# Optimization experiments

Measured on AMD Instinct MI355X. Metric: run time of the kernel, lower is better.

Reference implementation:

```python
import jax, jax.numpy as jnp
import numpy as np

N_NODES = 20000
E_RAND = 300000
IN_F, OUT_F, HEADS = 1280, 128, 4
HID = OUT_F * HEADS  # 512


def gat_conv(x, src, dst, W, attn_l, attn_r, bias, n_nodes):
    """DGL GATConv: fc (no bias) -> per-edge LeakyReLU(el_src+er_dst) ->
    segment softmax over incoming edges -> weighted scatter-sum -> +bias.
    Returns (N, HEADS, OUT_F)."""
    h = (x @ W).reshape(n_nodes, HEADS, OUT_F)            # (N,H,F)
    el = jnp.einsum('nhf,hf->nh', h, attn_l)              # (N,H)
    er = jnp.einsum('nhf,hf->nh', h, attn_r)              # (N,H)
    e = jax.nn.leaky_relu(el[src] + er[dst], 0.2)         # (E,H)
    emax = jax.ops.segment_max(e, dst, num_segments=n_nodes)
    ee = jnp.exp(e - emax[dst])                           # (E,H)
    denom = jax.ops.segment_sum(ee, dst, num_segments=n_nodes)
    alpha = ee / denom[dst]                               # (E,H)
    msg = h[src] * alpha[:, :, None]                      # (E,H,F)
    out = jax.ops.segment_sum(msg, dst, num_segments=n_nodes)
    return out + bias.reshape(HEADS, OUT_F)


def setup_inputs() -> dict:
    key = jax.random.key(0)
    ks = jax.random.split(key, 12)
    src_r = jax.random.randint(ks[0], (E_RAND,), 0, N_NODES)
    dst_r = jax.random.randint(ks[1], (E_RAND,), 0, N_NODES)
    self_loop = jnp.arange(N_NODES)
    src = jnp.concatenate([src_r, self_loop])  # self loops: contact[i][i]=1
    dst = jnp.concatenate([dst_r, self_loop])
    feature = jax.random.normal(ks[2], (N_NODES, IN_F), dtype=jnp.float32)
    s1 = 1.0 / np.sqrt(IN_F)
    s2 = 1.0 / np.sqrt(HID)
    return {
        'feature': feature,
        'W1': jax.random.normal(ks[3], (IN_F, HID), dtype=jnp.float32) * s1,
        'al1': jax.random.normal(ks[4], (HEADS, OUT_F), dtype=jnp.float32) * s2,
        'ar1': jax.random.normal(ks[5], (HEADS, OUT_F), dtype=jnp.float32) * s2,
        'b1': jnp.zeros((HID,), dtype=jnp.float32),
        'W2': jax.random.normal(ks[6], (HID, HID), dtype=jnp.float32) * s2,
        'al2': jax.random.normal(ks[7], (HEADS, OUT_F), dtype=jnp.float32) * s2,
        'ar2': jax.random.normal(ks[8], (HEADS, OUT_F), dtype=jnp.float32) * s2,
        'b2': jnp.zeros((HID,), dtype=jnp.float32),
        'Wfc': jax.random.normal(ks[9], (HID, 64), dtype=jnp.float32) * s2,
        'bfc': jnp.zeros((64,), dtype=jnp.float32),
        'src': src,
        'dst': dst,
    }


def reference(feature, W1, al1, ar1, b1, W2, al2, ar2, b2, Wfc, bfc, src, dst):
    n = feature.shape[0]
    out = gat_conv(feature, src, dst, W1, al1, ar1, b1, n)   # (N,4,128)
    out = jax.nn.elu(out).reshape(n, HID)                    # (N,512)
    out = gat_conv(out, src, dst, W2, al2, ar2, b2, n)       # (N,4,128)
    out = jax.nn.elu(out).reshape(n, HID)                    # (N,512)
    out = out @ Wfc + bfc                                    # (N,64)
    out = jax.nn.elu(out[None, :, :])                        # (1,N,64)
    return out
```

## Files before the change

### kernel.cpp

```cpp
#include <hip/hip_runtime.h>
#include <hip/hip_bf16.h>
#include <math.h>

#define HID 512
#define HEADS 4
#define OUTF 128

typedef __attribute__((ext_vector_type(8))) _Float16 f16x8_t;
typedef __attribute__((ext_vector_type(4))) _Float16 f16x4_t;
typedef __attribute__((ext_vector_type(4))) float f32x4_t;

__device__ __forceinline__ void gl_lds16(const void* g, void* l) {
    __builtin_amdgcn_global_load_lds(
        (const __attribute__((address_space(1))) void*)g,
        (__attribute__((address_space(3))) void*)l, 16, 0, 0);
}

__device__ __forceinline__ void stage_plane32(const _Float16* g, int strideE,
    int rbase, int rmax, char* plane, int wave, int lane)
{
    int gci = wave * 64 + lane;
    int r = gci >> 2, c = gci & 3;
    int rg = rbase + r; if (rg > rmax) rg = rmax;
    const char* s = (const char*)(g + (size_t)rg * strideE) + ((c ^ ((r >> 1) & 3)) << 4);
    char* d = plane + wave * 1024;
    gl_lds16(s, d);
}

__global__ __launch_bounds__(256) void conv16_kernel(const float* __restrict__ in,
    _Float16* __restrict__ o, int nquad)
{
    int stride = gridDim.x * 256;
    for (int i = blockIdx.x * 256 + threadIdx.x; i < nquad; i += stride) {
        float4 v = *(const float4*)&in[(size_t)i * 4];
        f16x4_t ov;
        ov[0] = (_Float16)v.x; ov[1] = (_Float16)v.y;
        ov[2] = (_Float16)v.z; ov[3] = (_Float16)v.w;
        *(f16x4_t*)&o[(size_t)i * 4] = ov;
    }
}

__global__ __launch_bounds__(256) void prep_w(const float* __restrict__ W,
    _Float16* __restrict__ Wt, int K, int NC)
{
    __shared__ float tile[32][33];
    const int k0 = blockIdx.x * 32, n0 = blockIdx.y * 32;
    const int t = threadIdx.x;
    {
        int r = t >> 3, c4 = (t & 7) * 4;
        float4 v = *(const float4*)&W[(size_t)(k0 + r) * NC + n0 + c4];
        tile[r][c4] = v.x; tile[r][c4 + 1] = v.y;
        tile[r][c4 + 2] = v.z; tile[r][c4 + 3] = v.w;
    }
    __syncthreads();
    int n = t >> 3, kc = (t & 7) * 4;
#pragma unroll
    for (int i = 0; i < 4; ++i)
        Wt[(size_t)(n0 + n) * K + k0 + kc + i] = (_Float16)tile[kc + i][n];
}

template<int EPI, int OUT16, int ELER>
__global__ __launch_bounds__(512, 6) void gemm_f16(
    const _Float16* __restrict__ Af, const _Float16* __restrict__ Bt,
    const float* __restrict__ bias,
    const float* __restrict__ attl, const float* __restrict__ attr,
    float* __restrict__ elp, float* __restrict__ erp,
    void* __restrict__ Cout, int M, int K, int NCOL, int ldC)
{
    __shared__ char lds[32768];
    const int tid = threadIdx.x;
    const int wave = tid >> 6, lane = tid & 63;
    const int wm = wave >> 2, wn = wave & 3;
    const int bm = blockIdx.y * 128, bn = blockIdx.x * 128;
    const int l15 = lane & 15, l4 = lane >> 4;
    const int swz = (l15 >> 1) & 3;

    f32x4_t acc[4][2];
#pragma unroll
    for (int i = 0; i < 4; ++i)
#pragma unroll
        for (int j = 0; j < 2; ++j) acc[i][j] = (f32x4_t){0.f, 0.f, 0.f, 0.f};

    const int nt = K >> 5;
    stage_plane32(Af, K, bm, M - 1, lds, wave, lane);
    stage_plane32(Bt, K, bn, NCOL - 1, lds + 8192, wave, lane);
    __syncthreads();

    for (int t = 0; t < nt; ++t) {
        char* AH = lds + (t & 1) * 16384;
        char* BH = AH + 8192;
        if (t + 1 < nt) {
            char* AHn = lds + ((t + 1) & 1) * 16384;
            stage_plane32(Af + (t + 1) * 32, K, bm, M - 1, AHn, wave, lane);
            stage_plane32(Bt + (t + 1) * 32, K, bn, NCOL - 1, AHn + 8192, wave, lane);
        }
        f16x8_t fa[4], fb[2];
#pragma unroll
        for (int mf = 0; mf < 4; ++mf) {
            int row = wm * 64 + mf * 16 + l15;
            fa[mf] = *(const f16x8_t*)(AH + row * 64 + ((l4 ^ swz) << 4));
        }
#pragma unroll
        for (int nf = 0; nf < 2; ++nf) {
            int rn = wn * 32 + nf * 16 + l15;
            fb[nf] = *(const f16x8_t*)(BH + rn * 64 + ((l4 ^ swz) << 4));
        }
#pragma unroll
        for (int mf = 0; mf < 4; ++mf)
#pragma unroll
            for (int nf = 0; nf < 2; ++nf)
                acc[mf][nf] = __builtin_amdgcn_mfma_f32_16x16x32_f16(fa[mf], fb[nf], acc[mf][nf], 0, 0, 0);
        __syncthreads();
    }
#pragma unroll
    for (int mf = 0; mf < 4; ++mf) {
        int rbase = bm + wm * 64 + mf * 16 + l4 * 4;
#pragma unroll
        for (int nf = 0; nf < 2; ++nf) {
            int col = bn + wn * 32 + nf * 16 + l15;
            if (col >= NCOL) continue;
#pragma unroll
            for (int r = 0; r < 4; ++r) {
                int row = rbase + r;
                if (row < M) {
                    float v = acc[mf][nf][r];
                    if (EPI) {
                        v += bias[col];
                        v = v > 0.f ? v : (expf(v) - 1.f);
                    }
                    if (OUT16) ((_Float16*)Cout)[(size_t)row * ldC + col] = (_Float16)v;
                    else       ((float*)Cout)[(size_t)row * ldC + col] = v;
                }
            }
        }
    }
    if (ELER) {
        const int head = blockIdx.x;
        float alv[2], arv[2];
#pragma unroll
        for (int nf = 0; nf < 2; ++nf) {
            int cl = wn * 32 + nf * 16 + l15;
            alv[nf] = attl[head * OUTF + cl];
            arv[nf] = attr[head * OUTF + cl];
        }
        float pel[4][4], perr[4][4];
#pragma unroll
        for (int mf = 0; mf < 4; ++mf)
#pragma unroll
            for (int r = 0; r < 4; ++r) {
                float se = 0.f, sr = 0.f;
#pragma unroll
                for (int nf = 0; nf < 2; ++nf) {
                    se = fmaf(acc[mf][nf][r], alv[nf], se);
                    sr = fmaf(acc[mf][nf][r], arv[nf], sr);
                }
                pel[mf][r] = se; perr[mf][r] = sr;
            }
#pragma unroll
        for (int off = 1; off < 16; off <<= 1)
#pragma unroll
            for (int mf = 0; mf < 4; ++mf)
#pragma unroll
                for (int r = 0; r < 4; ++r) {
                    pel[mf][r]  += __shfl_xor(pel[mf][r],  off);
                    perr[mf][r] += __shfl_xor(perr[mf][r], off);
                }
        __syncthreads();
        float* red = (float*)lds;
        if (l15 == 0) {
#pragma unroll
            for (int mf = 0; mf < 4; ++mf)
#pragma unroll
                for (int r = 0; r < 4; ++r) {
                    int rl = wm * 64 + mf * 16 + l4 * 4 + r;
                    red[rl * 4 + wn]       = pel[mf][r];
                    red[512 + rl * 4 + wn] = perr[mf][r];
                }
        }
        __syncthreads();
        if (tid < 128) {
            int row = bm + tid;
            if (row < M) {
                float es = red[tid * 4] + red[tid * 4 + 1] + red[tid * 4 + 2] + red[tid * 4 + 3];
                float rs = red[512 + tid * 4] + red[512 + tid * 4 + 1]
                         + red[512 + tid * 4 + 2] + red[512 + tid * 4 + 3];
                elp[row * HEADS + head] = es;
                erp[row * HEADS + head] = rs;
            }
        }
    }
}

__global__ void hist_kernel(const int* __restrict__ dst, int* __restrict__ deg, int E)
{
    int e = blockIdx.x * 256 + threadIdx.x;
    if (e < E) atomicAdd(&deg[dst[e]], 1);
}

__global__ __launch_bounds__(256) void scan1_kernel(const int* __restrict__ deg,
    int* __restrict__ offs, int* __restrict__ bsum, int N)
{
    __shared__ int buf[256];
    int tid = threadIdx.x;
    int i = blockIdx.x * 256 + tid;
    int v = (i < N) ? deg[i] : 0;
    buf[tid] = v;
    __syncthreads();
#pragma unroll
    for (int off = 1; off < 256; off <<= 1) {
        int t = (tid >= off) ? buf[tid - off] : 0;
        __syncthreads();
        buf[tid] += t;
        __syncthreads();
    }
    if (i < N) offs[i] = buf[tid] - v;
    if (tid == 255) bsum[blockIdx.x] = buf[255];
}

__global__ void scan2_kernel(int* __restrict__ bsum, int nb)
{
    if (threadIdx.x == 0) {
        int acc = 0;
        for (int b = 0; b < nb; ++b) { int t = bsum[b]; bsum[b] = acc; acc += t; }
        bsum[nb] = acc;
    }
}

__global__ void scan3_kernel(int* __restrict__ offs, const int* __restrict__ bsum,
                             int N, int nb)
{
    int i = blockIdx.x * 256 + threadIdx.x;
    if (i < N) offs[i] += bsum[blockIdx.x];
    if (i == 0) offs[N] = bsum[nb];
}

__global__ void fill_kernel(const int* __restrict__ srcv, const int* __restrict__ dstv,
    const int* __restrict__ offs, int* __restrict__ cursor,
    int* __restrict__ psrc, int E)
{
    int e = blockIdx.x * 256 + threadIdx.x;
    if (e < E) {
        int d = dstv[e];
        int p = atomicAdd(&cursor[d], 1);
        psrc[offs[d] + p] = srcv[e];
    }
}

__global__ __launch_bounds__(64) void aggregate_kernel(const _Float16* __restrict__ h,
    const int* __restrict__ offs, const int* __restrict__ psrc,
    const float* __restrict__ el, const float* __restrict__ er,
    const float* __restrict__ bias, _Float16* __restrict__ xo, int N)
{
    __shared__ int ssm[64];
    __shared__ float wsm[4][64];
    int n = blockIdx.x;
    int lane = threadIdx.x;
    int c = lane * 8;
    int head = lane >> 4;
    float4 erv = *(const float4*)&er[n * HEADS];
    float acc[8];
#pragma unroll
    for (int k = 0; k < 8; ++k) acc[k] = 0.f;
    float ws = 0.f;
    int beg = offs[n], end = offs[n + 1];
    for (int base = beg; base < end; base += 64) {
        int cnt = min(64, end - base);
        if (lane < cnt) {
            int s = psrc[base + lane];
            float4 lv = *(const float4*)&el[s * HEADS];
            float x;
            x = lv.x + erv.x; x = x > 0.f ? x : 0.2f * x; wsm[0][lane] = expf(x);
            x = lv.y + erv.y; x = x > 0.f ? x : 0.2f * x; wsm[1][lane] = expf(x);
            x = lv.z + erv.z; x = x > 0.f ? x : 0.2f * x; wsm[2][lane] = expf(x);
            x = lv.w + erv.w; x = x > 0.f ? x : 0.2f * x; wsm[3][lane] = expf(x);
            ssm[lane] = s;
        }
        __syncthreads();
        int j = 0;
        for (; j + 4 <= cnt; j += 4) {
            int s0 = ssm[j], s1 = ssm[j + 1], s2 = ssm[j + 2], s3 = ssm[j + 3];
            float w0 = wsm[head][j],     w1 = wsm[head][j + 1];
            float w2 = wsm[head][j + 2], w3 = wsm[head][j + 3];
            f16x8_t v0 = *(const f16x8_t*)&h[(size_t)s0 * HID + c];
            f16x8_t v1 = *(const f16x8_t*)&h[(size_t)s1 * HID + c];
            f16x8_t v2 = *(const f16x8_t*)&h[(size_t)s2 * HID + c];
            f16x8_t v3 = *(const f16x8_t*)&h[(size_t)s3 * HID + c];
#pragma unroll
            for (int k = 0; k < 8; ++k) {
                acc[k] = fmaf(w0, (float)v0[k], acc[k]);
                acc[k] = fmaf(w1, (float)v1[k], acc[k]);
                acc[k] = fmaf(w2, (float)v2[k], acc[k]);
                acc[k] = fmaf(w3, (float)v3[k], acc[k]);
            }
            ws += w0 + w1 + w2 + w3;
        }
        for (; j < cnt; ++j) {
            int s0 = ssm[j];
            float w0 = wsm[head][j];
            f16x8_t v0 = *(const f16x8_t*)&h[(size_t)s0 * HID + c];
#pragma unroll
            for (int k = 0; k < 8; ++k) acc[k] = fmaf(w0, (float)v0[k], acc[k]);
            ws += w0;
        }
        __syncthreads();
    }
    float inv = 1.f / ws;
    float4 b0 = *(const float4*)&bias[c];
    float4 b1 = *(const float4*)&bias[c + 4];
    float bb[8] = {b0.x, b0.y, b0.z, b0.w, b1.x, b1.y, b1.z, b1.w};
    f16x8_t ov;
#pragma unroll
    for (int k = 0; k < 8; ++k) {
        float r = acc[k] * inv + bb[k];
        r = r > 0.f ? r : (expf(r) - 1.f);
        ov[k] = (_Float16)r;
    }
    *(f16x8_t*)&xo[(size_t)n * HID + c] = ov;
}

extern "C" void kernel_launch(void* const* d_in, const int* in_sizes, int n_in,
                              void* d_out, int out_size, void* d_ws, size_t ws_size,
                              hipStream_t stream)
{
    const float* feature = (const float*)d_in[0];
    const float* W1  = (const float*)d_in[1];
    const float* al1 = (const float*)d_in[2];
    const float* ar1 = (const float*)d_in[3];
    const float* b1  = (const float*)d_in[4];
    const float* W2  = (const float*)d_in[5];
    const float* al2 = (const float*)d_in[6];
    const float* ar2 = (const float*)d_in[7];
    const float* b2  = (const float*)d_in[8];
    const float* Wfc = (const float*)d_in[9];
    const float* bfc = (const float*)d_in[10];
    const int* src = (const int*)d_in[11];
    const int* dst = (const int*)d_in[12];
    const int N = in_sizes[0] / 1280;
    const int E = in_sizes[11];
    const int nb = (N + 255) / 256;
    float* out = (float*)d_out;

    char* ws = (char*)d_ws;
    size_t off = 0;
    auto alloc = [&](size_t bytes) {
        void* p = ws + off;
        off += (bytes + 255) & ~(size_t)255;
        return p;
    };
    int* deg    = (int*)alloc((size_t)N * 4);
    int* cursor = (int*)alloc((size_t)N * 4);
    int* offs   = (int*)alloc((size_t)(N + 1) * 4);
    int* bsum   = (int*)alloc((size_t)(nb + 1) * 4);
    float* el   = (float*)alloc((size_t)N * HEADS * 4);
    float* er   = (float*)alloc((size_t)N * HEADS * 4);
    int* psrc   = (int*)alloc((size_t)E * 4);
    _Float16* featf = (_Float16*)alloc((size_t)N * 1280 * 2);
    _Float16* hbuf  = (_Float16*)alloc((size_t)N * HID * 2);
    _Float16* xh    = (_Float16*)alloc((size_t)N * HID * 2);
    _Float16* W1t   = (_Float16*)alloc((size_t)HID * 1280 * 2);
    _Float16* W2t   = (_Float16*)alloc((size_t)HID * HID * 2);
    _Float16* Wft   = (_Float16*)alloc((size_t)64 * HID * 2);

    hipMemsetAsync(deg, 0, (size_t)N * 4, stream);
    hipMemsetAsync(cursor, 0, (size_t)N * 4, stream);
    hist_kernel<<<(E + 255) / 256, 256, 0, stream>>>(dst, deg, E);
    scan1_kernel<<<nb, 256, 0, stream>>>(deg, offs, bsum, N);
    scan2_kernel<<<1, 64, 0, stream>>>(bsum, nb);
    scan3_kernel<<<nb, 256, 0, stream>>>(offs, bsum, N, nb);
    fill_kernel<<<(E + 255) / 256, 256, 0, stream>>>(src, dst, offs, cursor, psrc, E);

    conv16_kernel<<<2048, 256, 0, stream>>>(feature, featf, N * 1280 / 4);
    prep_w<<<dim3(1280 / 32, HID / 32), 256, 0, stream>>>(W1, W1t, 1280, HID);
    prep_w<<<dim3(HID / 32, HID / 32), 256, 0, stream>>>(W2, W2t, HID, HID);
    prep_w<<<dim3(HID / 32, 64 / 32), 256, 0, stream>>>(Wfc, Wft, HID, 64);

    dim3 ggrid(HID / 128, (N + 127) / 128);
    dim3 fgrid(1, (N + 127) / 128);

    gemm_f16<0, 1, 1><<<ggrid, 512, 0, stream>>>(featf, W1t, nullptr,
                                                 al1, ar1, el, er,
                                                 hbuf, N, 1280, HID, HID);
    aggregate_kernel<<<N, 64, 0, stream>>>(hbuf, offs, psrc, el, er, b1, xh, N);

    gemm_f16<0, 1, 1><<<ggrid, 512, 0, stream>>>(xh, W2t, nullptr,
                                                 al2, ar2, el, er,
                                                 hbuf, N, HID, HID, HID);
    aggregate_kernel<<<N, 64, 0, stream>>>(hbuf, offs, psrc, el, er, b2, xh, N);

    gemm_f16<1, 0, 0><<<fgrid, 512, 0, stream>>>(xh, Wft, bfc,
                                                 nullptr, nullptr, nullptr, nullptr,
                                                 out, N, HID, 64, 64);
}
```

Baseline: 276.1 us.

## Use 4-wave GEMM blocks with 64x64 warp tiles and XCD-aware block remapping

Switches the f16 GEMM from 8 waves per 128x128 tile to 4 waves, each computing a 64x64 sub-tile (4x4 MFMA fragments). Each wave reuses its fragments across more MFMAs and the block issues fewer LDS reads. The grid is also flattened to 1D and block IDs are remapped so consecutive logical tiles land on the same XCD, which should improve L2 reuse of shared A rows across the column tiles. In exchange it uses more accumulator registers per thread and fewer waves per CU to hide latency.

```diff
diff --git a/kernel.cpp b/kernel.cpp
--- a/kernel.cpp
+++ b/kernel.cpp
@@ -17,14 +17,17 @@
 }
 
 __device__ __forceinline__ void stage_plane32(const _Float16* g, int strideE,
-    int rbase, int rmax, char* plane, int wave, int lane)
-{
-    int gci = wave * 64 + lane;
-    int r = gci >> 2, c = gci & 3;
-    int rg = rbase + r; if (rg > rmax) rg = rmax;
-    const char* s = (const char*)(g + (size_t)rg * strideE) + ((c ^ ((r >> 1) & 3)) << 4);
-    char* d = plane + wave * 1024;
-    gl_lds16(s, d);
+    int rbase, int rmax, char* plane, int tid)
+{
+#pragma unroll
+    for (int j = 0; j < 2; ++j) {
+        int gci = j * 256 + tid;
+        int r = gci >> 2, c = gci & 3;
+        int rg = rbase + r; if (rg > rmax) rg = rmax;
+        const char* s = (const char*)(g + (size_t)rg * strideE) + ((c ^ ((r >> 1) & 3)) << 4);
+        char* d = plane + (j * 256 + (tid & ~63)) * 16;
+        gl_lds16(s, d);
+    }
 }
 
 __global__ __launch_bounds__(256) void conv16_kernel(const float* __restrict__ in,
@@ -60,30 +63,36 @@
 }
 
 template<int EPI, int OUT16, int ELER>
-__global__ __launch_bounds__(512, 6) void gemm_f16(
+__global__ __launch_bounds__(256, 3) void gemm_f16(
     const _Float16* __restrict__ Af, const _Float16* __restrict__ Bt,
     const float* __restrict__ bias,
     const float* __restrict__ attl, const float* __restrict__ attr,
     float* __restrict__ elp, float* __restrict__ erp,
-    void* __restrict__ Cout, int M, int K, int NCOL, int ldC)
+    void* __restrict__ Cout, int M, int K, int NCOL, int ldC,
+    int ncolT, int nwg)
 {
     __shared__ char lds[32768];
     const int tid = threadIdx.x;
     const int wave = tid >> 6, lane = tid & 63;
-    const int wm = wave >> 2, wn = wave & 3;
-    const int bm = blockIdx.y * 128, bn = blockIdx.x * 128;
+    const int wm = wave >> 1, wn = wave & 1;
+    const int b = blockIdx.x;
+    const int q = nwg >> 3, rr = nwg & 7;
+    const int xcd = b & 7, ib = b >> 3;
+    const int logical = (xcd < rr ? xcd * (q + 1) : rr * (q + 1) + (xcd - rr) * q) + ib;
+    const int bm = (logical / ncolT) * 128, bcol = logical % ncolT;
+    const int bn = bcol * 128;
     const int l15 = lane & 15, l4 = lane >> 4;
     const int swz = (l15 >> 1) & 3;
 
-    f32x4_t acc[4][2];
+    f32x4_t acc[4][4];
 #pragma unroll
     for (int i = 0; i < 4; ++i)
 #pragma unroll
-        for (int j = 0; j < 2; ++j) acc[i][j] = (f32x4_t){0.f, 0.f, 0.f, 0.f};
+        for (int j = 0; j < 4; ++j) acc[i][j] = (f32x4_t){0.f, 0.f, 0.f, 0.f};
 
     const int nt = K >> 5;
-    stage_plane32(Af, K, bm, M - 1, lds, wave, lane);
-    stage_plane32(Bt, K, bn, NCOL - 1, lds + 8192, wave, lane);
+    stage_plane32(Af, K, bm, M - 1, lds, tid);
+    stage_plane32(Bt, K, bn, NCOL - 1, lds + 8192, tid);
     __syncthreads();
 
     for (int t = 0; t < nt; ++t) {
@@ -91,24 +100,24 @@
         char* BH = AH + 8192;
         if (t + 1 < nt) {
             char* AHn = lds + ((t + 1) & 1) * 16384;
-            stage_plane32(Af + (t + 1) * 32, K, bm, M - 1, AHn, wave, lane);
-            stage_plane32(Bt + (t + 1) * 32, K, bn, NCOL - 1, AHn + 8192, wave, lane);
-        }
-        f16x8_t fa[4], fb[2];
+            stage_plane32(Af + (t + 1) * 32, K, bm, M - 1, AHn, tid);
+            stage_plane32(Bt + (t + 1) * 32, K, bn, NCOL - 1, AHn + 8192, tid);
+        }
+        f16x8_t fa[4], fb[4];
 #pragma unroll
         for (int mf = 0; mf < 4; ++mf) {
             int row = wm * 64 + mf * 16 + l15;
             fa[mf] = *(const f16x8_t*)(AH + row * 64 + ((l4 ^ swz) << 4));
         }
 #pragma unroll
-        for (int nf = 0; nf < 2; ++nf) {
-            int rn = wn * 32 + nf * 16 + l15;
+        for (int nf = 0; nf < 4; ++nf) {
+            int rn = wn * 64 + nf * 16 + l15;
             fb[nf] = *(const f16x8_t*)(BH + rn * 64 + ((l4 ^ swz) << 4));
         }
 #pragma unroll
         for (int mf = 0; mf < 4; ++mf)
 #pragma unroll
-            for (int nf = 0; nf < 2; ++nf)
+            for (int nf = 0; nf < 4; ++nf)
                 acc[mf][nf] = __builtin_amdgcn_mfma_f32_16x16x32_f16(fa[mf], fb[nf], acc[mf][nf], 0, 0, 0);
         __syncthreads();
     }
@@ -116,8 +125,8 @@
     for (int mf = 0; mf < 4; ++mf) {
         int rbase = bm + wm * 64 + mf * 16 + l4 * 4;
 #pragma unroll
-        for (int nf = 0; nf < 2; ++nf) {
-            int col = bn + wn * 32 + nf * 16 + l15;
+        for (int nf = 0; nf < 4; ++nf) {
+            int col = bn + wn * 64 + nf * 16 + l15;
             if (col >= NCOL) continue;
 #pragma unroll
             for (int r = 0; r < 4; ++r) {
@@ -135,11 +144,11 @@
         }
     }
     if (ELER) {
-        const int head = blockIdx.x;
-        float alv[2], arv[2];
-#pragma unroll
-        for (int nf = 0; nf < 2; ++nf) {
-            int cl = wn * 32 + nf * 16 + l15;
+        const int head = bcol;
+        float alv[4], arv[4];
+#pragma unroll
+        for (int nf = 0; nf < 4; ++nf) {
+            int cl = wn * 64 + nf * 16 + l15;
             alv[nf] = attl[head * OUTF + cl];
             arv[nf] = attr[head * OUTF + cl];
         }
@@ -150,7 +159,7 @@
             for (int r = 0; r < 4; ++r) {
                 float se = 0.f, sr = 0.f;
 #pragma unroll
-                for (int nf = 0; nf < 2; ++nf) {
+                for (int nf = 0; nf < 4; ++nf) {
                     se = fmaf(acc[mf][nf][r], alv[nf], se);
                     sr = fmaf(acc[mf][nf][r], arv[nf], sr);
                 }
@@ -173,17 +182,16 @@
 #pragma unroll
                 for (int r = 0; r < 4; ++r) {
                     int rl = wm * 64 + mf * 16 + l4 * 4 + r;
-                    red[rl * 4 + wn]       = pel[mf][r];
-                    red[512 + rl * 4 + wn] = perr[mf][r];
+                    red[rl * 2 + wn]       = pel[mf][r];
+                    red[256 + rl * 2 + wn] = perr[mf][r];
                 }
         }
         __syncthreads();
         if (tid < 128) {
             int row = bm + tid;
             if (row < M) {
-                float es = red[tid * 4] + red[tid * 4 + 1] + red[tid * 4 + 2] + red[tid * 4 + 3];
-                float rs = red[512 + tid * 4] + red[512 + tid * 4 + 1]
-                         + red[512 + tid * 4 + 2] + red[512 + tid * 4 + 3];
+                float es = red[tid * 2] + red[tid * 2 + 1];
+                float rs = red[256 + tid * 2] + red[256 + tid * 2 + 1];
                 elp[row * HEADS + head] = es;
                 erp[row * HEADS + head] = rs;
             }
@@ -374,20 +382,24 @@
     prep_w<<<dim3(HID / 32, HID / 32), 256, 0, stream>>>(W2, W2t, HID, HID);
     prep_w<<<dim3(HID / 32, 64 / 32), 256, 0, stream>>>(Wfc, Wft, HID, 64);
 
-    dim3 ggrid(HID / 128, (N + 127) / 128);
-    dim3 fgrid(1, (N + 127) / 128);
-
-    gemm_f16<0, 1, 1><<<ggrid, 512, 0, stream>>>(featf, W1t, nullptr,
-                                                 al1, ar1, el, er,
-                                                 hbuf, N, 1280, HID, HID);
+    const int nrowT = (N + 127) / 128;
+    const int nwgG = nrowT * (HID / 128);
+    const int nwgF = nrowT;
+
+    gemm_f16<0, 1, 1><<<nwgG, 256, 0, stream>>>(featf, W1t, nullptr,
+                                                al1, ar1, el, er,
+                                                hbuf, N, 1280, HID, HID,
+                                                HID / 128, nwgG);
     aggregate_kernel<<<N, 64, 0, stream>>>(hbuf, offs, psrc, el, er, b1, xh, N);
 
-    gemm_f16<0, 1, 1><<<ggrid, 512, 0, stream>>>(xh, W2t, nullptr,
-                                                 al2, ar2, el, er,
-                                                 hbuf, N, HID, HID, HID);
+    gemm_f16<0, 1, 1><<<nwgG, 256, 0, stream>>>(xh, W2t, nullptr,
+                                                al2, ar2, el, er,
+                                                hbuf, N, HID, HID, HID,
+                                                HID / 128, nwgG);
     aggregate_kernel<<<N, 64, 0, stream>>>(hbuf, offs, psrc, el, er, b2, xh, N);
 
-    gemm_f16<1, 0, 0><<<fgrid, 512, 0, stream>>>(xh, Wft, bfc,
-                                                 nullptr, nullptr, nullptr, nullptr,
-                                                 out, N, HID, 64, 64);
-}
+    gemm_f16<1, 0, 0><<<nwgF, 256, 0, stream>>>(xh, Wft, bfc,
+                                                nullptr, nullptr, nullptr, nullptr,
+                                                out, N, HID, 64, 64,
+                                                1, nwgF);
+}
```

Measured after the change: 262.0 us. 1.05x faster.
